# Kernel optimization log

Hardware: AMD Instinct MI355X
Metric: run time of the kernel (lower is better)

Reference implementation:

```python
import jax, jax.numpy as jnp
import numpy as np

NUM_EMBEDDINGS = 1024
EMBEDDING_DIM = 64
COMMITMENT_WEIGHT = 0.25
BATCH = 262144


def setup_inputs() -> dict:
    key = jax.random.key(0)
    k1, k2 = jax.random.split(key)
    z = jax.random.normal(k1, (BATCH, EMBEDDING_DIM), dtype=jnp.float32)
    # torch init: uniform_(-1/K, 1/K)
    bound = 1.0 / NUM_EMBEDDINGS
    codebook = jax.random.uniform(k2, (NUM_EMBEDDINGS, EMBEDDING_DIM), dtype=jnp.float32,
                                  minval=-bound, maxval=bound)
    return {"z": z, "codebook": codebook}


def reference(z, codebook):
    # distances[b, k] = ||z_b||^2 - 2 z_b . c_k + ||c_k||^2   -> [B, K]
    z2 = jnp.sum(z * z, axis=1, keepdims=True)                 # [B, 1]
    c2 = jnp.sum(codebook * codebook, axis=1)                  # [K]
    cross = jnp.matmul(z, codebook.T)                          # [B, K]
    distances = z2 - 2.0 * cross + c2
    indices = jnp.argmin(distances, axis=1)                    # [B]
    # original uses one-hot @ codebook; direct gather is the same math
    z_q = codebook[indices]                                    # [B, D]
    commitment_loss = jnp.mean((jax.lax.stop_gradient(z_q) - z) ** 2)
    codebook_loss = jnp.mean((z_q - jax.lax.stop_gradient(z)) ** 2)
    vq_loss = codebook_loss + COMMITMENT_WEIGHT * commitment_loss
    # straight-through estimator
    z_q_st = z + jax.lax.stop_gradient(z_q - z)
    return z_q_st, vq_loss, indices
```

## Files before the change

### kernel.cpp

```cpp
#include <hip/hip_runtime.h>

#define BATCH   262144
#define NCODE   1024
#define DIM     64
#define BLOCK   256
#define NBLK    (BATCH / BLOCK)
#define MARGIN  4e-5f
#define QCAP    65536


typedef __attribute__((ext_vector_type(8))) short bf16x8;
typedef __attribute__((ext_vector_type(4))) float f32x4;

#define MFMA(a, b, c) __builtin_amdgcn_mfma_f32_16x16x32_bf16(a, b, c, 0, 0, 0)

__global__ void c2_kernel(const float* __restrict__ cb, float* __restrict__ c2,
                          unsigned int* __restrict__ qcount) {
    int k = blockIdx.x * blockDim.x + threadIdx.x;
    if (k == 0) *qcount = 0u;
    if (k >= NCODE) return;
    const float* row = cb + (size_t)k * DIM;
    float r[8];
#pragma unroll
    for (int j = 0; j < 8; ++j) r[j] = __fmul_rn(row[j], row[j]);
#pragma unroll
    for (int i = 8; i < DIM; i += 8) {
#pragma unroll
        for (int j = 0; j < 8; ++j) r[j] = __fadd_rn(r[j], __fmul_rn(row[i + j], row[i + j]));
    }
    c2[k] = __fadd_rn(__fadd_rn(__fadd_rn(r[0], r[1]), __fadd_rn(r[2], r[3])),
                      __fadd_rn(__fadd_rn(r[4], r[5]), __fadd_rn(r[6], r[7])));
}

__global__ void cbt_kernel(const float* __restrict__ cb, float* __restrict__ cbT) {
    const int gid = blockIdx.x * blockDim.x + threadIdx.x;
    const int k = gid >> 6, d = gid & 63;
    cbT[(size_t)d * NCODE + k] = cb[gid];
}

__device__ __forceinline__ void split1(float f, unsigned short& h, unsigned short& l) {
    unsigned u = __float_as_uint(f);
    unsigned r = (u + 0x7fffu + ((u >> 16) & 1u)) >> 16;
    h = (unsigned short)r;
    float hf = __uint_as_float(r << 16);
    float lo = f - hf;
    unsigned u2 = __float_as_uint(lo);
    l = (unsigned short)((u2 + 0x7fffu + ((u2 >> 16) & 1u)) >> 16);
}

__global__ void pack_kernel(const float* __restrict__ cb, unsigned short* __restrict__ pack) {
    const int tid  = blockIdx.x * blockDim.x + threadIdx.x;
    const int t    = tid >> 6, lane = tid & 63;
    const int c    = t * 16 + (lane & 15);
    const int g    = lane >> 4;
#pragma unroll
    for (int s = 0; s < 2; ++s) {
        const float* src = cb + (size_t)c * DIM + s * 32 + g * 8;
        bf16x8 hv, lv;
#pragma unroll
        for (int j = 0; j < 8; ++j) {
            unsigned short hh, ll; split1(src[j], hh, ll);
            hv[j] = (short)hh; lv[j] = (short)ll;
        }
        *(bf16x8*)(pack + ((size_t)(t * 4 + 2 * s + 0) * 64 + lane) * 8) = hv;
        *(bf16x8*)(pack + ((size_t)(t * 4 + 2 * s + 1) * 64 + lane) * 8) = lv;
    }
}

__global__ __launch_bounds__(256) void screen_kernel(
        const float* __restrict__ z, const unsigned short* __restrict__ pack,
        const float* __restrict__ c2, float* __restrict__ out_idx,
        unsigned char* __restrict__ flags, int* __restrict__ queue,
        unsigned int* __restrict__ qcount)
{
    __shared__ unsigned short lds[16384];
    const int tid  = threadIdx.x;
    const int lane = tid & 63, wid = tid >> 6;
    const int col  = lane & 15, g = lane >> 4;
    const int rowbase = blockIdx.x * 128 + wid * 32;

    bf16x8 Ah[2][2], Al[2][2];
#pragma unroll
    for (int rt = 0; rt < 2; ++rt)
#pragma unroll
        for (int s = 0; s < 2; ++s) {
            const float* zp = z + (size_t)(rowbase + rt * 16 + col) * DIM + s * 32 + g * 8;
            float tmp[8];
            *(float4*)(tmp)     = ((const float4*)zp)[0];
            *(float4*)(tmp + 4) = ((const float4*)zp)[1];
            bf16x8 hv, lv;
#pragma unroll
            for (int j = 0; j < 8; ++j) {
                unsigned short hh, ll; split1(tmp[j], hh, ll);
                hv[j] = (short)hh; lv[j] = (short)ll;
            }
            Ah[rt][s] = hv; Al[rt][s] = lv;
        }

    float b1[8], b2[8], bk[8];
#pragma unroll
    for (int i = 0; i < 8; ++i) { b1[i] = __builtin_inff(); b2[i] = __builtin_inff(); bk[i] = 0.f; }
    float codef = (float)col;

#define UPD(i, sv) { const float s_ = (sv); const bool lt = s_ < b1[i]; \
                     b2[i] = fminf(b2[i], fmaxf(s_, b1[i])); \
                     bk[i] = lt ? codef : bk[i]; \
                     b1[i] = fminf(b1[i], s_); }

#pragma unroll 1
    for (int chunk = 0; chunk < 8; ++chunk) {
        if (chunk) __syncthreads();
        {
            const unsigned short* gs = pack + (size_t)chunk * 16384;
#pragma unroll
            for (int i = 0; i < 8; ++i) {
                const int seg = wid * 8 + i;
                bf16x8 v = *(const bf16x8*)(gs + seg * 512 + lane * 8);
                *(bf16x8*)(lds + seg * 512 + lane * 8) = v;
            }
        }
        float c2r[8];
#pragma unroll
        for (int tt = 0; tt < 8; ++tt) c2r[tt] = c2[(chunk * 8 + tt) * 16 + col];
        __syncthreads();
#pragma unroll
        for (int tt = 0; tt < 8; ++tt) {
            const unsigned short* lb = lds + tt * 2048;
            bf16x8 Bh0 = *(const bf16x8*)(lb +    0 + lane * 8);
            bf16x8 Bl0 = *(const bf16x8*)(lb +  512 + lane * 8);
            bf16x8 Bh1 = *(const bf16x8*)(lb + 1024 + lane * 8);
            bf16x8 Bl1 = *(const bf16x8*)(lb + 1536 + lane * 8);
            const float c2v = c2r[tt];
            f32x4 acc0 = {0.f, 0.f, 0.f, 0.f}, acc1 = {0.f, 0.f, 0.f, 0.f};
            acc0 = MFMA(Ah[0][0], Bh0, acc0); acc0 = MFMA(Ah[0][1], Bh1, acc0);
            acc0 = MFMA(Ah[0][0], Bl0, acc0); acc0 = MFMA(Al[0][0], Bh0, acc0);
            acc0 = MFMA(Ah[0][1], Bl1, acc0); acc0 = MFMA(Al[0][1], Bh1, acc0);
            acc1 = MFMA(Ah[1][0], Bh0, acc1); acc1 = MFMA(Ah[1][1], Bh1, acc1);
            acc1 = MFMA(Ah[1][0], Bl0, acc1); acc1 = MFMA(Al[1][0], Bh0, acc1);
            acc1 = MFMA(Ah[1][1], Bl1, acc1); acc1 = MFMA(Al[1][1], Bh1, acc1);
#pragma unroll
            for (int reg = 0; reg < 4; ++reg) {
                UPD(reg,     __fmaf_rn(-2.0f, acc0[reg], c2v));
                UPD(4 + reg, __fmaf_rn(-2.0f, acc1[reg], c2v));
            }
            codef += 16.f;
        }
    }
#undef UPD

#pragma unroll
    for (int i = 0; i < 8; ++i) {
        float v1 = b1[i], v2 = b2[i], vk = bk[i];
#pragma unroll
        for (int m = 1; m < 16; m <<= 1) {
            const float o1 = __shfl_xor(v1, m);
            const float o2 = __shfl_xor(v2, m);
            const float ok = __shfl_xor(vk, m);
            v2 = fminf(fminf(v2, o2), fmaxf(v1, o1));
            if (o1 < v1) vk = ok;
            v1 = fminf(v1, o1);
        }
        if (col == 0) {
            const int rt = i >> 2, reg = i & 3;
            const int row = rowbase + rt * 16 + g * 4 + reg;
            out_idx[row] = vk;
            const bool f = (v2 - v1 <= MARGIN);
            flags[row] = f ? 1 : 0;
            if (f) {
                unsigned int p = atomicAdd(qcount, 1u);
                if (p < QCAP) queue[p] = row;
            }
        }
    }
}

__device__ void fix_row(int row, const float* __restrict__ z, const float* __restrict__ cbT,
                        const float* __restrict__ c2, float* __restrict__ out_idx,
                        float* zs, float* rv, int* ri)
{
    const int tid = threadIdx.x;
    __syncthreads();
    if (tid < 16) ((float4*)zs)[tid] = ((const float4*)(z + (size_t)row * DIM))[tid];
    __syncthreads();
    float ra[8];
#pragma unroll
    for (int j = 0; j < 8; ++j) ra[j] = __fmul_rn(zs[j], zs[j]);
#pragma unroll
    for (int d = 8; d < DIM; d += 8) {
#pragma unroll
        for (int j = 0; j < 8; ++j) ra[j] = __fadd_rn(ra[j], __fmul_rn(zs[d + j], zs[d + j]));
    }
    const float z2 = __fadd_rn(__fadd_rn(__fadd_rn(ra[0], ra[1]), __fadd_rn(ra[2], ra[3])),
                               __fadd_rn(__fadd_rn(ra[4], ra[5]), __fadd_rn(ra[6], ra[7])));
    float a[4] = {0.f, 0.f, 0.f, 0.f};
#pragma unroll 8
    for (int d = 0; d < DIM; ++d) {
        const float zd = zs[d];
        const float4 cv = ((const float4*)(cbT + (size_t)d * NCODE))[tid];
        a[0] = __fmaf_rn(zd, cv.x, a[0]);
        a[1] = __fmaf_rn(zd, cv.y, a[1]);
        a[2] = __fmaf_rn(zd, cv.z, a[2]);
        a[3] = __fmaf_rn(zd, cv.w, a[3]);
    }
    const int k0 = tid * 4;
    float best = __builtin_inff();
    int bestk = NCODE;
#pragma unroll
    for (int j = 0; j < 4; ++j) {
        const float dist = __fadd_rn(__fmaf_rn(-2.0f, a[j], z2), c2[k0 + j]);
        if (dist < best) { best = dist; bestk = k0 + j; }
    }
    rv[tid] = best; ri[tid] = bestk;
    __syncthreads();
#pragma unroll
    for (int s = 128; s > 0; s >>= 1) {
        if (tid < s) {
            const float ov = rv[tid + s]; const int oi = ri[tid + s];
            if (ov < rv[tid] || (ov == rv[tid] && oi < ri[tid])) { rv[tid] = ov; ri[tid] = oi; }
        }
        __syncthreads();
    }
    if (tid == 0) out_idx[row] = (float)ri[0];
}

__global__ __launch_bounds__(256) void fix_kernel(
        const float* __restrict__ z, const float* __restrict__ cbT,
        const float* __restrict__ c2, const int* __restrict__ queue,
        const unsigned int* __restrict__ qcount, const unsigned char* __restrict__ flags,
        float* __restrict__ out_idx)
{
    __shared__ float zs[DIM];
    __shared__ float rv[256];
    __shared__ int   ri[256];
    const unsigned int nq = *qcount;
    if (nq <= QCAP) {
        for (unsigned int qi = blockIdx.x; qi < nq; qi += gridDim.x)
            fix_row(queue[qi], z, cbT, c2, out_idx, zs, rv, ri);
    } else {
        for (int row = blockIdx.x; row < BATCH; row += (int)gridDim.x)
            if (flags[row]) fix_row(row, z, cbT, c2, out_idx, zs, rv, ri);
    }
}

__global__ __launch_bounds__(BLOCK) void emit_kernel(
        const float* __restrict__ z, const float* __restrict__ cb,
        const float* __restrict__ out_idx, float* __restrict__ out_zq,
        double* __restrict__ partial)
{
    const int b = blockIdx.x * BLOCK + threadIdx.x;
    const int bestk = (int)out_idx[b];
    const float* cq = cb + (size_t)bestk * DIM;
    const float4* zv = (const float4*)(z + (size_t)b * DIM);
    const float4* qv = (const float4*)cq;
    float4* ov = (float4*)(out_zq + (size_t)b * DIM);
    double lsum = 0.0;
#pragma unroll
    for (int i = 0; i < DIM / 4; ++i) {
        float4 qq = qv[i], zl = zv[i];
        float qa[4] = {qq.x, qq.y, qq.z, qq.w};
        float za[4] = {zl.x, zl.y, zl.z, zl.w};
        float o[4];
#pragma unroll
        for (int j = 0; j < 4; ++j) {
            const float t = __fsub_rn(qa[j], za[j]);
            o[j] = __fadd_rn(za[j], t);
            lsum += (double)t * (double)t;
        }
        float4 vv; vv.x = o[0]; vv.y = o[1]; vv.z = o[2]; vv.w = o[3];
        ov[i] = vv;
    }

    __shared__ double sred[BLOCK];
    sred[threadIdx.x] = lsum;
    __syncthreads();
#pragma unroll
    for (int s = BLOCK / 2; s > 0; s >>= 1) {
        if (threadIdx.x < s) sred[threadIdx.x] += sred[threadIdx.x + s];
        __syncthreads();
    }
    if (threadIdx.x == 0) partial[blockIdx.x] = sred[0];
}

__global__ void loss_kernel(const double* __restrict__ partial, float* __restrict__ out_loss) {
    __shared__ double sred[256];
    double s = 0.0;
    for (int i = threadIdx.x; i < NBLK; i += 256) s += partial[i];
    sred[threadIdx.x] = s;
    __syncthreads();
#pragma unroll
    for (int st = 128; st > 0; st >>= 1) {
        if (threadIdx.x < st) sred[threadIdx.x] += sred[threadIdx.x + st];
        __syncthreads();
    }
    if (threadIdx.x == 0) {
        const double mean = sred[0] / (double)((size_t)BATCH * DIM);
        const float L = (float)mean;
        out_loss[0] = __fadd_rn(L, __fmul_rn(0.25f, L));
    }
}

extern "C" void kernel_launch(void* const* d_in, const int* in_sizes, int n_in,
                              void* d_out, int out_size, void* d_ws, size_t ws_size,
                              hipStream_t stream) {
    (void)in_sizes; (void)n_in; (void)out_size; (void)ws_size;
    const float* z  = (const float*)d_in[0];
    const float* cb = (const float*)d_in[1];
    float* out      = (float*)d_out;
    float* out_zq   = out;
    float* out_loss = out + (size_t)BATCH * DIM;
    float* out_idx  = out + (size_t)BATCH * DIM + 1;
    double* partial = (double*)d_ws;
    float* c2       = (float*)((char*)d_ws + 8192);
    unsigned int* qcount = (unsigned int*)((char*)d_ws + 12288);
    unsigned char* flags = (unsigned char*)d_ws + 12544;
    unsigned short* pack = (unsigned short*)((char*)d_ws + 274688);
    int* queue      = (int*)((char*)d_ws + 536832);
    float* cbT      = (float*)((char*)d_ws + 798976);

    c2_kernel<<<NCODE / 256, 256, 0, stream>>>(cb, c2, qcount);
    cbt_kernel<<<256, 256, 0, stream>>>(cb, cbT);
    pack_kernel<<<16, 256, 0, stream>>>(cb, pack);
    screen_kernel<<<BATCH / 128, 256, 0, stream>>>(z, pack, c2, out_idx, flags, queue, qcount);
    fix_kernel<<<2048, 256, 0, stream>>>(z, cbT, c2, queue, qcount, flags, out_idx);
    emit_kernel<<<NBLK, BLOCK, 0, stream>>>(z, cb, out_idx, out_zq, partial);
    loss_kernel<<<1, 256, 0, stream>>>(partial, out_loss);
}
```

Baseline: 314.8 us.

## Fuse codebook prep kernels and widen screen tile, reading codebook from global

Merges the three codebook preprocessing kernels (norms, transpose, bf16 hi/lo pack) into one launch. The screening kernel now handles 64 rows per wave instead of 32, halving the grid, and reads packed codebook fragments straight from global/L2 instead of staging them in shared memory with barriers. The top-2 update uses a med3 instruction to track the second-best distance more cheaply. More rows per wave raises register pressure (more A fragments and 16 top-2 slots) and may lower occupancy, and dropping LDS staging relies on cache hits for the shared codebook.

```diff
diff --git a/kernel.cpp b/kernel.cpp
--- a/kernel.cpp
+++ b/kernel.cpp
@@ -13,30 +13,6 @@
 typedef __attribute__((ext_vector_type(4))) float f32x4;
 
 #define MFMA(a, b, c) __builtin_amdgcn_mfma_f32_16x16x32_bf16(a, b, c, 0, 0, 0)
-
-__global__ void c2_kernel(const float* __restrict__ cb, float* __restrict__ c2,
-                          unsigned int* __restrict__ qcount) {
-    int k = blockIdx.x * blockDim.x + threadIdx.x;
-    if (k == 0) *qcount = 0u;
-    if (k >= NCODE) return;
-    const float* row = cb + (size_t)k * DIM;
-    float r[8];
-#pragma unroll
-    for (int j = 0; j < 8; ++j) r[j] = __fmul_rn(row[j], row[j]);
-#pragma unroll
-    for (int i = 8; i < DIM; i += 8) {
-#pragma unroll
-        for (int j = 0; j < 8; ++j) r[j] = __fadd_rn(r[j], __fmul_rn(row[i + j], row[i + j]));
-    }
-    c2[k] = __fadd_rn(__fadd_rn(__fadd_rn(r[0], r[1]), __fadd_rn(r[2], r[3])),
-                      __fadd_rn(__fadd_rn(r[4], r[5]), __fadd_rn(r[6], r[7])));
-}
-
-__global__ void cbt_kernel(const float* __restrict__ cb, float* __restrict__ cbT) {
-    const int gid = blockIdx.x * blockDim.x + threadIdx.x;
-    const int k = gid >> 6, d = gid & 63;
-    cbT[(size_t)d * NCODE + k] = cb[gid];
-}
 
 __device__ __forceinline__ void split1(float f, unsigned short& h, unsigned short& l) {
     unsigned u = __float_as_uint(f);
@@ -48,22 +24,43 @@
     l = (unsigned short)((u2 + 0x7fffu + ((u2 >> 16) & 1u)) >> 16);
 }
 
-__global__ void pack_kernel(const float* __restrict__ cb, unsigned short* __restrict__ pack) {
-    const int tid  = blockIdx.x * blockDim.x + threadIdx.x;
-    const int t    = tid >> 6, lane = tid & 63;
-    const int c    = t * 16 + (lane & 15);
-    const int g    = lane >> 4;
-#pragma unroll
-    for (int s = 0; s < 2; ++s) {
-        const float* src = cb + (size_t)c * DIM + s * 32 + g * 8;
-        bf16x8 hv, lv;
-#pragma unroll
-        for (int j = 0; j < 8; ++j) {
-            unsigned short hh, ll; split1(src[j], hh, ll);
-            hv[j] = (short)hh; lv[j] = (short)ll;
-        }
-        *(bf16x8*)(pack + ((size_t)(t * 4 + 2 * s + 0) * 64 + lane) * 8) = hv;
-        *(bf16x8*)(pack + ((size_t)(t * 4 + 2 * s + 1) * 64 + lane) * 8) = lv;
+__global__ __launch_bounds__(256) void prep_kernel(
+        const float* __restrict__ cb, float* __restrict__ c2,
+        float* __restrict__ cbT, unsigned short* __restrict__ pack,
+        unsigned int* __restrict__ qcount)
+{
+    const int gid = blockIdx.x * 256 + threadIdx.x;
+    if (gid == 0) *qcount = 0u;
+    cbT[(size_t)(gid & 63) * NCODE + (gid >> 6)] = cb[gid];
+    if (gid < NCODE) {
+        const float* row = cb + (size_t)gid * DIM;
+        float r[8];
+#pragma unroll
+        for (int j = 0; j < 8; ++j) r[j] = __fmul_rn(row[j], row[j]);
+#pragma unroll
+        for (int i = 8; i < DIM; i += 8) {
+#pragma unroll
+            for (int j = 0; j < 8; ++j) r[j] = __fadd_rn(r[j], __fmul_rn(row[i + j], row[i + j]));
+        }
+        c2[gid] = __fadd_rn(__fadd_rn(__fadd_rn(r[0], r[1]), __fadd_rn(r[2], r[3])),
+                            __fadd_rn(__fadd_rn(r[4], r[5]), __fadd_rn(r[6], r[7])));
+    }
+    if (gid < 4096) {
+        const int t = gid >> 6, lane = gid & 63;
+        const int c = t * 16 + (lane & 15);
+        const int g = lane >> 4;
+#pragma unroll
+        for (int s = 0; s < 2; ++s) {
+            const float* src = cb + (size_t)c * DIM + s * 32 + g * 8;
+            bf16x8 hv, lv;
+#pragma unroll
+            for (int j = 0; j < 8; ++j) {
+                unsigned short hh, ll; split1(src[j], hh, ll);
+                hv[j] = (short)hh; lv[j] = (short)ll;
+            }
+            *(bf16x8*)(pack + ((size_t)(t * 4 + 2 * s + 0) * 64 + lane) * 8) = hv;
+            *(bf16x8*)(pack + ((size_t)(t * 4 + 2 * s + 1) * 64 + lane) * 8) = lv;
+        }
     }
 }
 
@@ -73,15 +70,14 @@
         unsigned char* __restrict__ flags, int* __restrict__ queue,
         unsigned int* __restrict__ qcount)
 {
-    __shared__ unsigned short lds[16384];
     const int tid  = threadIdx.x;
     const int lane = tid & 63, wid = tid >> 6;
     const int col  = lane & 15, g = lane >> 4;
-    const int rowbase = blockIdx.x * 128 + wid * 32;
-
-    bf16x8 Ah[2][2], Al[2][2];
-#pragma unroll
-    for (int rt = 0; rt < 2; ++rt)
+    const int rowbase = blockIdx.x * 256 + wid * 64;
+
+    bf16x8 Ah[4][2], Al[4][2];
+#pragma unroll
+    for (int rt = 0; rt < 4; ++rt)
 #pragma unroll
         for (int s = 0; s < 2; ++s) {
             const float* zp = z + (size_t)(rowbase + rt * 16 + col) * DIM + s * 32 + g * 8;
@@ -97,51 +93,39 @@
             Ah[rt][s] = hv; Al[rt][s] = lv;
         }
 
-    float b1[8], b2[8], bk[8];
-#pragma unroll
-    for (int i = 0; i < 8; ++i) { b1[i] = __builtin_inff(); b2[i] = __builtin_inff(); bk[i] = 0.f; }
+    float b1[16], b2[16], bk[16];
+#pragma unroll
+    for (int i = 0; i < 16; ++i) { b1[i] = __builtin_inff(); b2[i] = __builtin_inff(); bk[i] = 0.f; }
     float codef = (float)col;
 
-#define UPD(i, sv) { const float s_ = (sv); const bool lt = s_ < b1[i]; \
-                     b2[i] = fminf(b2[i], fmaxf(s_, b1[i])); \
-                     bk[i] = lt ? codef : bk[i]; \
+#define UPD(i, sv) { const float s_ = (sv); \
+                     bk[i] = (s_ < b1[i]) ? codef : bk[i]; \
+                     b2[i] = __builtin_amdgcn_fmed3f(s_, b1[i], b2[i]); \
                      b1[i] = fminf(b1[i], s_); }
 
 #pragma unroll 1
-    for (int chunk = 0; chunk < 8; ++chunk) {
-        if (chunk) __syncthreads();
-        {
-            const unsigned short* gs = pack + (size_t)chunk * 16384;
-#pragma unroll
-            for (int i = 0; i < 8; ++i) {
-                const int seg = wid * 8 + i;
-                bf16x8 v = *(const bf16x8*)(gs + seg * 512 + lane * 8);
-                *(bf16x8*)(lds + seg * 512 + lane * 8) = v;
-            }
-        }
+    for (int t8 = 0; t8 < 8; ++t8) {
         float c2r[8];
 #pragma unroll
-        for (int tt = 0; tt < 8; ++tt) c2r[tt] = c2[(chunk * 8 + tt) * 16 + col];
-        __syncthreads();
-#pragma unroll
-        for (int tt = 0; tt < 8; ++tt) {
-            const unsigned short* lb = lds + tt * 2048;
-            bf16x8 Bh0 = *(const bf16x8*)(lb +    0 + lane * 8);
-            bf16x8 Bl0 = *(const bf16x8*)(lb +  512 + lane * 8);
-            bf16x8 Bh1 = *(const bf16x8*)(lb + 1024 + lane * 8);
-            bf16x8 Bl1 = *(const bf16x8*)(lb + 1536 + lane * 8);
-            const float c2v = c2r[tt];
-            f32x4 acc0 = {0.f, 0.f, 0.f, 0.f}, acc1 = {0.f, 0.f, 0.f, 0.f};
-            acc0 = MFMA(Ah[0][0], Bh0, acc0); acc0 = MFMA(Ah[0][1], Bh1, acc0);
-            acc0 = MFMA(Ah[0][0], Bl0, acc0); acc0 = MFMA(Al[0][0], Bh0, acc0);
-            acc0 = MFMA(Ah[0][1], Bl1, acc0); acc0 = MFMA(Al[0][1], Bh1, acc0);
-            acc1 = MFMA(Ah[1][0], Bh0, acc1); acc1 = MFMA(Ah[1][1], Bh1, acc1);
-            acc1 = MFMA(Ah[1][0], Bl0, acc1); acc1 = MFMA(Al[1][0], Bh0, acc1);
-            acc1 = MFMA(Ah[1][1], Bl1, acc1); acc1 = MFMA(Al[1][1], Bh1, acc1);
-#pragma unroll
-            for (int reg = 0; reg < 4; ++reg) {
-                UPD(reg,     __fmaf_rn(-2.0f, acc0[reg], c2v));
-                UPD(4 + reg, __fmaf_rn(-2.0f, acc1[reg], c2v));
+        for (int u = 0; u < 8; ++u) c2r[u] = c2[(t8 * 8 + u) * 16 + col];
+#pragma unroll
+        for (int u = 0; u < 8; ++u) {
+            const unsigned short* bp = pack + (size_t)(t8 * 8 + u) * 2048;
+            bf16x8 Bh0 = *(const bf16x8*)(bp +    0 + lane * 8);
+            bf16x8 Bl0 = *(const bf16x8*)(bp +  512 + lane * 8);
+            bf16x8 Bh1 = *(const bf16x8*)(bp + 1024 + lane * 8);
+            bf16x8 Bl1 = *(const bf16x8*)(bp + 1536 + lane * 8);
+            const float c2v = c2r[u];
+#pragma unroll
+            for (int rt = 0; rt < 4; ++rt) {
+                f32x4 acc = {0.f, 0.f, 0.f, 0.f};
+                acc = MFMA(Ah[rt][0], Bh0, acc); acc = MFMA(Ah[rt][1], Bh1, acc);
+                acc = MFMA(Ah[rt][0], Bl0, acc); acc = MFMA(Al[rt][0], Bh0, acc);
+                acc = MFMA(Ah[rt][1], Bl1, acc); acc = MFMA(Al[rt][1], Bh1, acc);
+#pragma unroll
+                for (int reg = 0; reg < 4; ++reg) {
+                    UPD(rt * 4 + reg, __fmaf_rn(-2.0f, acc[reg], c2v));
+                }
             }
             codef += 16.f;
         }
@@ -149,7 +133,7 @@
 #undef UPD
 
 #pragma unroll
-    for (int i = 0; i < 8; ++i) {
+    for (int i = 0; i < 16; ++i) {
         float v1 = b1[i], v2 = b2[i], vk = bk[i];
 #pragma unroll
         for (int m = 1; m < 16; m <<= 1) {
@@ -317,10 +301,8 @@
     int* queue      = (int*)((char*)d_ws + 536832);
     float* cbT      = (float*)((char*)d_ws + 798976);
 
-    c2_kernel<<<NCODE / 256, 256, 0, stream>>>(cb, c2, qcount);
-    cbt_kernel<<<256, 256, 0, stream>>>(cb, cbT);
-    pack_kernel<<<16, 256, 0, stream>>>(cb, pack);
-    screen_kernel<<<BATCH / 128, 256, 0, stream>>>(z, pack, c2, out_idx, flags, queue, qcount);
+    prep_kernel<<<256, 256, 0, stream>>>(cb, c2, cbT, pack, qcount);
+    screen_kernel<<<BATCH / 256, 256, 0, stream>>>(z, pack, c2, out_idx, flags, queue, qcount);
     fix_kernel<<<2048, 256, 0, stream>>>(z, cbT, c2, queue, qcount, flags, out_idx);
     emit_kernel<<<NBLK, BLOCK, 0, stream>>>(z, cb, out_idx, out_zq, partial);
     loss_kernel<<<1, 256, 0, stream>>>(partial, out_loss);
```

After: 340.7 us. 8.2% more time.
